# Kernel tuning notes

Measured on AMD Instinct MI355X. Metric: run time of the kernel, lower is better.

The kernel has to match this reference:

```python
import jax, jax.numpy as jnp
import numpy as np

UNITS = 64

def _tri_indices(u):
    # pairs (a,b) with b>=a in row-major order == tf.boolean_mask(product_mask1)
    pairs = [(a, b) for a in range(u) for b in range(a, u)]
    ia = np.array([p[0] for p in pairs], np.int32)
    ib = np.array([p[1] for p in pairs], np.int32)
    # triples: for product1 index p=(a,b), keep c>=b (derived from mask2 loops)
    ip, ic = [], []
    for p, (a, b) in enumerate(pairs):
        for c in range(b, u):
            ip.append(p)
            ic.append(c)
    return ia, ib, np.array(ip, np.int32), np.array(ic, np.int32)

def setup_inputs() -> dict:
    key = jax.random.key(0)
    k0, k1, k2, k3, k4 = jax.random.split(key, 5)
    B, D, u = 4096, 66, UNITS
    nprod1 = u * (u + 1) // 2            # 2080
    nprod2 = u * (u + 1) * (u + 2) // 6  # 45760
    inputs = jax.random.normal(k0, (B, D), jnp.float32)
    fw1 = jax.random.uniform(k1, (u,), jnp.float32, 0.0, 2.0 * np.pi * 40.0)
    fw2 = jax.random.normal(k2, (u,), jnp.float32) * 0.05
    fb1 = jax.random.normal(k3, (u,), jnp.float32) * 0.05
    wo = jax.random.normal(k4, (u + nprod1 + nprod2, u), jnp.float32) * 0.05
    return {"inputs": inputs, "fw1": fw1, "fw2": fw2, "fb1": fb1, "wo": wo}

def reference(inputs, fw1, fw2, fb1, wo):
    u = fw1.shape[0]
    ia, ib, ip, ic = _tri_indices(u)
    # Fourier features: cos(x * w1 + b1) * w2,  [B, u]
    f = jnp.cos(inputs[:, :u] * fw1 + fb1) * fw2
    # quadratic upper-triangular products, [B, nprod1] (gather instead of dense outer+mask)
    p1 = f[:, ia] * f[:, ib]
    # cubic products c>=b>=a, [B, nprod2]
    p2 = p1[:, ip] * f[:, ic]
    comb = jnp.concatenate([f, p1, p2], axis=1)  # [B, u+nprod1+nprod2]
    pad = jnp.zeros((inputs.shape[0], inputs.shape[1] - u), inputs.dtype)
    return jnp.concatenate([comb @ wo, pad], axis=1) + inputs
```

## Files before the change

kernel.cpp:

```cpp
#include <hip/hip_runtime.h>
#include <hip/hip_bf16.h>

#define NB      4096
#define ND      66
#define NSTEPP  1792
#define KS      64
#define CH      28
#define MB      32
#define FS      72

#define SBLK    NSTEPP
#define FBLK    (NB*FS/256)
#define PBLK    32

typedef __attribute__((ext_vector_type(8))) _Float16 f16x8;
typedef __attribute__((ext_vector_type(4))) _Float16 f16x4;
typedef __attribute__((ext_vector_type(4))) float    f32x4;

__device__ __attribute__((aligned(16))) _Float16 g_f[NB * FS];
__device__ __attribute__((aligned(16))) _Float16 g_woTi[(size_t)(NSTEPP + 1) * 2048];
__device__ __attribute__((aligned(16))) _Float16 g_part[(size_t)KS * MB * 8192];

__constant__ int c_bb[8] = {0, 48, 204, 532, 1096, 1960, 3188, 4844};

__device__ inline unsigned octet_desc(int o) {
    int t = 0;
#pragma unroll
    for (int i = 1; i < 8; ++i) t += (o >= c_bb[i]);
    int li = o - c_bb[t];
    int P = 8 * t + 8, T = P * (P + 1) / 2;
    int s0, s1;
    if (li == 0)       { s0 = 64; s1 = 64; }
    else if (li <= P)  { s0 = li - 1; s1 = 64; }
    else if (li <= P + T) {
        int r = li - P - 1, a = 0;
        while (r >= P - a) { r -= P - a; ++a; }
        s0 = a; s1 = a + r;
    } else             { s0 = 65; s1 = 65; }
    return (unsigned)s0 | ((unsigned)s1 << 8) | ((unsigned)(8 * t) << 16);
}

__global__ void k_prep(const float* __restrict__ inp, const float* __restrict__ fw1,
                       const float* __restrict__ fw2, const float* __restrict__ fb1,
                       const float* __restrict__ wo, float* __restrict__ out) {
    const int bid = blockIdx.x, tid = threadIdx.x;
    if (bid < SBLK) {
        __shared__ unsigned sd[4];
        if (tid < 4) sd[tid] = octet_desc(bid * 4 + tid);
        __syncthreads();
        const int q = tid >> 6, gg = (tid >> 4) & 3, rl = tid & 15;
        const unsigned d = sd[gg];
        const int s0 = d & 255, s1 = (d >> 8) & 255, cb = d >> 16;
        const int n = q * 16 + rl;
        f16x8 v;
        if (s0 == 64) {
#pragma unroll
            for (int j = 0; j < 8; ++j) v[j] = (_Float16)wo[(cb + j) * 64 + n];
        } else if (s0 < 64 && s1 == 64) {
            int base = 64 + s0 * (129 - s0) / 2 + (cb - s0);
#pragma unroll
            for (int j = 0; j < 8; ++j)
                v[j] = (cb + j >= s0) ? (_Float16)wo[(base + j) * 64 + n] : (_Float16)0.f;
        } else if (s0 < 64) {
            int a = s0, b = s1;
            int TP = 45760 - (64 - a) * (65 - a) * (66 - a) / 6;
            int RB = b * (129 - b) / 2 - a * (129 - a) / 2;
            int base = 2144 + TP + RB + (cb - b);
#pragma unroll
            for (int j = 0; j < 8; ++j)
                v[j] = (cb + j >= b) ? (_Float16)wo[(base + j) * 64 + n] : (_Float16)0.f;
        } else {
#pragma unroll
            for (int j = 0; j < 8; ++j) v[j] = (_Float16)0.f;
        }
        *(f16x8*)(g_woTi + (size_t)bid * 2048 + tid * 8) = v;
    } else if (bid < SBLK + FBLK) {
        int i = (bid - SBLK) * 256 + tid;
        int r = i / FS, c = i - r * FS;
        float v;
        if (c < 64)       v = cosf(inp[r * ND + c] * fw1[c] + fb1[c]) * fw2[c];
        else if (c == 64) v = 1.0f;
        else              v = 0.0f;
        g_f[i] = (_Float16)v;
    } else {
        int i = (bid - SBLK - FBLK) * 256 + tid;
        int r = i >> 1, c = 64 + (i & 1);
        out[r * ND + c] = inp[r * ND + c];
    }
}

__global__ __launch_bounds__(128, 4) void k_gemm() {
    __shared__ __attribute__((aligned(16))) _Float16 fl[128 * FS];
    __shared__ __attribute__((aligned(16))) unsigned ldescT[4 * 32];
    const int mb = blockIdx.x, ks = blockIdx.y, tid = threadIdx.x;
    const int s0c = ks * CH;

    {
        const uint4* src = (const uint4*)(g_f + (size_t)mb * 128 * FS);
        uint4* dst = (uint4*)fl;
        for (int e = tid; e < 128 * FS * 2 / 16; e += 128) dst[e] = src[e];
        {
            int gg = tid >> 5, s = tid & 31;
            ldescT[tid] = (s < CH) ? octet_desc((s0c + s) * 4 + gg) : (65u | (65u << 8));
        }
    }
    __syncthreads();

    const int wave = tid >> 6, lane = tid & 63, rl = lane & 15, g = lane >> 4;
    const _Float16* fr0 = fl + (wave * 64 +  0 + rl) * FS;
    const _Float16* fr1 = fl + (wave * 64 + 16 + rl) * FS;
    const _Float16* fr2 = fl + (wave * 64 + 32 + rl) * FS;
    const _Float16* fr3 = fl + (wave * 64 + 48 + rl) * FS;

    f32x4 acc[4][4];
#pragma unroll
    for (int a = 0; a < 4; ++a)
#pragma unroll
        for (int q = 0; q < 4; ++q) acc[a][q] = f32x4{0.f, 0.f, 0.f, 0.f};

    f16x8 c0{}, c1{}, c2{}, c3{};
    _Float16 fa0 = 0, fa1 = 0, fa2 = 0, fa3 = 0;
    int cbPrev = -1, siPrev = -1;

    const _Float16* bptr = g_woTi + (size_t)s0c * 2048 + lane * 8;
    f16x8 B0 = *(const f16x8*)(bptr +    0);
    f16x8 B1 = *(const f16x8*)(bptr +  512);
    f16x8 B2 = *(const f16x8*)(bptr + 1024);
    f16x8 B3 = *(const f16x8*)(bptr + 1536);
    bptr += 2048;

#define STEP(dv)                                                               \
    {                                                                          \
        const int si0 = (dv) & 255, si1 = ((dv) >> 8) & 255;                   \
        const int cb = __builtin_amdgcn_readfirstlane((dv) >> 16);             \
        if (__any(si0 != siPrev)) {                                            \
            siPrev = si0;                                                      \
            fa0 = fr0[si0]; fa1 = fr1[si0]; fa2 = fr2[si0]; fa3 = fr3[si0];    \
        }                                                                      \
        if (cb != cbPrev) {                                                    \
            cbPrev = cb;                                                       \
            c0 = *(const f16x8*)(fr0 + cb); c1 = *(const f16x8*)(fr1 + cb);    \
            c2 = *(const f16x8*)(fr2 + cb); c3 = *(const f16x8*)(fr3 + cb);    \
        }                                                                      \
        f16x8 nB0 = *(const f16x8*)(bptr +    0);                              \
        f16x8 nB1 = *(const f16x8*)(bptr +  512);                              \
        f16x8 nB2 = *(const f16x8*)(bptr + 1024);                              \
        f16x8 nB3 = *(const f16x8*)(bptr + 1536);                              \
        bptr += 2048;                                                          \
        const _Float16 p0 = fa0 * fr0[si1], p1 = fa1 * fr1[si1];               \
        const _Float16 p2 = fa2 * fr2[si1], p3 = fa3 * fr3[si1];               \
        const f16x8 a0 = c0 * p0, a1 = c1 * p1, a2 = c2 * p2, a3 = c3 * p3;    \
        acc[0][0] = __builtin_amdgcn_mfma_f32_16x16x32_f16(a0, B0, acc[0][0], 0, 0, 0); \
        acc[0][1] = __builtin_amdgcn_mfma_f32_16x16x32_f16(a0, B1, acc[0][1], 0, 0, 0); \
        acc[0][2] = __builtin_amdgcn_mfma_f32_16x16x32_f16(a0, B2, acc[0][2], 0, 0, 0); \
        acc[0][3] = __builtin_amdgcn_mfma_f32_16x16x32_f16(a0, B3, acc[0][3], 0, 0, 0); \
        acc[1][0] = __builtin_amdgcn_mfma_f32_16x16x32_f16(a1, B0, acc[1][0], 0, 0, 0); \
        acc[1][1] = __builtin_amdgcn_mfma_f32_16x16x32_f16(a1, B1, acc[1][1], 0, 0, 0); \
        acc[1][2] = __builtin_amdgcn_mfma_f32_16x16x32_f16(a1, B2, acc[1][2], 0, 0, 0); \
        acc[1][3] = __builtin_amdgcn_mfma_f32_16x16x32_f16(a1, B3, acc[1][3], 0, 0, 0); \
        acc[2][0] = __builtin_amdgcn_mfma_f32_16x16x32_f16(a2, B0, acc[2][0], 0, 0, 0); \
        acc[2][1] = __builtin_amdgcn_mfma_f32_16x16x32_f16(a2, B1, acc[2][1], 0, 0, 0); \
        acc[2][2] = __builtin_amdgcn_mfma_f32_16x16x32_f16(a2, B2, acc[2][2], 0, 0, 0); \
        acc[2][3] = __builtin_amdgcn_mfma_f32_16x16x32_f16(a2, B3, acc[2][3], 0, 0, 0); \
        acc[3][0] = __builtin_amdgcn_mfma_f32_16x16x32_f16(a3, B0, acc[3][0], 0, 0, 0); \
        acc[3][1] = __builtin_amdgcn_mfma_f32_16x16x32_f16(a3, B1, acc[3][1], 0, 0, 0); \
        acc[3][2] = __builtin_amdgcn_mfma_f32_16x16x32_f16(a3, B2, acc[3][2], 0, 0, 0); \
        acc[3][3] = __builtin_amdgcn_mfma_f32_16x16x32_f16(a3, B3, acc[3][3], 0, 0, 0); \
        B0 = nB0; B1 = nB1; B2 = nB2; B3 = nB3;                                \
    }

    const unsigned* dT = ldescT + g * 32;
#pragma unroll 1
    for (int s2 = 0; s2 < CH; s2 += 2) {
        uint2 dd = *(const uint2*)(dT + s2);
        STEP(dd.x);
        STEP(dd.y);
    }
#undef STEP

    _Float16* pp = g_part + ((size_t)ks * MB + mb) * 8192 + wave * 4096;
#pragma unroll
    for (int a = 0; a < 4; ++a)
#pragma unroll
        for (int q = 0; q < 4; ++q) {
            f16x4 v;
            v[0] = (_Float16)acc[a][q][0]; v[1] = (_Float16)acc[a][q][1];
            v[2] = (_Float16)acc[a][q][2]; v[3] = (_Float16)acc[a][q][3];
            *(f16x4*)(pp + (a * 4 + q) * 256 + lane * 4) = v;
        }
}

__global__ void k_reduce(const float* __restrict__ inp, float* __restrict__ out) {
    int t = blockIdx.x * 256 + threadIdx.x;
    int c = t & 63, rg = t >> 6;
    int mb = rg >> 5, wave = (rg >> 4) & 1, a = (rg >> 2) & 3, g = rg & 3;
    int q = c >> 4, rl = c & 15, lane = g * 16 + rl;
    int rbase = mb * 128 + wave * 64 + a * 16 + g * 4;
    float acc[4];
#pragma unroll
    for (int i2 = 0; i2 < 4; ++i2) acc[i2] = inp[(rbase + i2) * ND + c];
    const _Float16* pp = g_part + (size_t)mb * 8192 + wave * 4096
                       + (a * 4 + q) * 256 + lane * 4;
#pragma unroll
    for (int ks = 0; ks < KS; ++ks) {
        const f16x4 p = *(const f16x4*)(pp + (size_t)ks * MB * 8192);
#pragma unroll
        for (int i2 = 0; i2 < 4; ++i2) acc[i2] += (float)p[i2];
    }
#pragma unroll
    for (int i2 = 0; i2 < 4; ++i2) out[(rbase + i2) * ND + c] = acc[i2];
}

extern "C" void kernel_launch(void* const* d_in, const int* in_sizes, int n_in,
                              void* d_out, int out_size, void* d_ws, size_t ws_size,
                              hipStream_t stream) {
    const float* inp = (const float*)d_in[0];
    const float* fw1 = (const float*)d_in[1];
    const float* fw2 = (const float*)d_in[2];
    const float* fb1 = (const float*)d_in[3];
    const float* wo  = (const float*)d_in[4];
    float* out = (float*)d_out;

    k_prep<<<SBLK + FBLK + PBLK, 256, 0, stream>>>(inp, fw1, fw2, fb1, wo, out);
    k_gemm<<<dim3(MB, KS), 128, 0, stream>>>();
    k_reduce<<<256, 256, 0, stream>>>(inp, out);
}
```

Baseline: 49.15 us.

## Halve K-split count and coalesce weight repack through shared-memory transpose

The GEMM K-split count drops from 64 to 32, with each block handling twice as many steps. This halves the fp16 partial-sum buffer written and later reduced, at the cost of fewer blocks in flight. The weight repack in the prep kernel now reads each row of wo as two contiguous float4 loads per thread instead of strided scalar loads. It then transposes the data in shared memory before one coalesced 16-byte store. The per-step descriptor table and the padded weight buffer are enlarged to match the longer chunk.

New measurement: 49.23 us. About the same (+0.2%).

```diff
diff --git a/kernel.cpp b/kernel.cpp
--- a/kernel.cpp
+++ b/kernel.cpp
@@ -4,8 +4,8 @@
 #define NB      4096
 #define ND      66
 #define NSTEPP  1792
-#define KS      64
-#define CH      28
+#define KS      32
+#define CH      56
 #define MB      32
 #define FS      72
 
@@ -18,7 +18,7 @@
 typedef __attribute__((ext_vector_type(4))) float    f32x4;
 
 __device__ __attribute__((aligned(16))) _Float16 g_f[NB * FS];
-__device__ __attribute__((aligned(16))) _Float16 g_woTi[(size_t)(NSTEPP + 1) * 2048];
+__device__ __attribute__((aligned(16))) _Float16 g_woTi[(size_t)(NSTEPP + 8) * 2048];
 __device__ __attribute__((aligned(16))) _Float16 g_part[(size_t)KS * MB * 8192];
 
 __constant__ int c_bb[8] = {0, 48, 204, 532, 1096, 1960, 3188, 4844};
@@ -45,35 +45,49 @@
                        const float* __restrict__ wo, float* __restrict__ out) {
     const int bid = blockIdx.x, tid = threadIdx.x;
     if (bid < SBLK) {
-        __shared__ unsigned sd[4];
-        if (tid < 4) sd[tid] = octet_desc(bid * 4 + tid);
+        __shared__ int sbrow[4], sminj[4];
+        __shared__ __attribute__((aligned(16))) _Float16 sw[2048];
+        if (tid < 4) {
+            unsigned d = octet_desc(bid * 4 + tid);
+            int s0 = d & 255, s1 = (d >> 8) & 255, cb = d >> 16;
+            int brow, minj = 0;
+            if (s0 == 64) {
+                brow = cb;
+            } else if (s0 < 64 && s1 == 64) {
+                brow = 64 + s0 * (129 - s0) / 2 + (cb - s0);
+                minj = (s0 > cb) ? s0 - cb : 0;
+            } else if (s0 < 64) {
+                int a = s0, b = s1;
+                int TP = 45760 - (64 - a) * (65 - a) * (66 - a) / 6;
+                int RB = b * (129 - b) / 2 - a * (129 - a) / 2;
+                brow = 2144 + TP + RB + (cb - b);
+                minj = (b > cb) ? b - cb : 0;
+            } else brow = -1;
+            sbrow[tid] = brow; sminj[tid] = minj;
+        }
         __syncthreads();
-        const int q = tid >> 6, gg = (tid >> 4) & 3, rl = tid & 15;
-        const unsigned d = sd[gg];
-        const int s0 = d & 255, s1 = (d >> 8) & 255, cb = d >> 16;
-        const int n = q * 16 + rl;
-        f16x8 v;
-        if (s0 == 64) {
-#pragma unroll
-            for (int j = 0; j < 8; ++j) v[j] = (_Float16)wo[(cb + j) * 64 + n];
-        } else if (s0 < 64 && s1 == 64) {
-            int base = 64 + s0 * (129 - s0) / 2 + (cb - s0);
-#pragma unroll
-            for (int j = 0; j < 8; ++j)
-                v[j] = (cb + j >= s0) ? (_Float16)wo[(base + j) * 64 + n] : (_Float16)0.f;
-        } else if (s0 < 64) {
-            int a = s0, b = s1;
-            int TP = 45760 - (64 - a) * (65 - a) * (66 - a) / 6;
-            int RB = b * (129 - b) / 2 - a * (129 - a) / 2;
-            int base = 2144 + TP + RB + (cb - b);
-#pragma unroll
-            for (int j = 0; j < 8; ++j)
-                v[j] = (cb + j >= b) ? (_Float16)wo[(base + j) * 64 + n] : (_Float16)0.f;
+        const int o = tid >> 6, l = tid & 63;
+        const int j = l >> 3, n0 = 8 * (l & 7);
+        const int brow = sbrow[o], minj = sminj[o];
+        f16x8 hv;
+        if (brow >= 0 && j >= minj) {
+            const float4 w0 = *(const float4*)(wo + (size_t)(brow + j) * 64 + n0);
+            const float4 w1 = *(const float4*)(wo + (size_t)(brow + j) * 64 + n0 + 4);
+            hv[0] = (_Float16)w0.x; hv[1] = (_Float16)w0.y;
+            hv[2] = (_Float16)w0.z; hv[3] = (_Float16)w0.w;
+            hv[4] = (_Float16)w1.x; hv[5] = (_Float16)w1.y;
+            hv[6] = (_Float16)w1.z; hv[7] = (_Float16)w1.w;
         } else {
 #pragma unroll
-            for (int j = 0; j < 8; ++j) v[j] = (_Float16)0.f;
-        }
-        *(f16x8*)(g_woTi + (size_t)bid * 2048 + tid * 8) = v;
+            for (int k = 0; k < 8; ++k) hv[k] = (_Float16)0.f;
+        }
+#pragma unroll
+        for (int k = 0; k < 8; ++k) {
+            int n = n0 + k;
+            sw[(n >> 4) * 512 + o * 128 + (n & 15) * 8 + j] = hv[k];
+        }
+        __syncthreads();
+        *(f16x8*)(g_woTi + (size_t)bid * 2048 + tid * 8) = *(const f16x8*)(sw + tid * 8);
     } else if (bid < SBLK + FBLK) {
         int i = (bid - SBLK) * 256 + tid;
         int r = i / FS, c = i - r * FS;
@@ -91,7 +105,7 @@
 
 __global__ __launch_bounds__(128, 4) void k_gemm() {
     __shared__ __attribute__((aligned(16))) _Float16 fl[128 * FS];
-    __shared__ __attribute__((aligned(16))) unsigned ldescT[4 * 32];
+    __shared__ __attribute__((aligned(16))) unsigned ldescT[4 * 64];
     const int mb = blockIdx.x, ks = blockIdx.y, tid = threadIdx.x;
     const int s0c = ks * CH;
 
@@ -99,9 +113,9 @@
         const uint4* src = (const uint4*)(g_f + (size_t)mb * 128 * FS);
         uint4* dst = (uint4*)fl;
         for (int e = tid; e < 128 * FS * 2 / 16; e += 128) dst[e] = src[e];
-        {
-            int gg = tid >> 5, s = tid & 31;
-            ldescT[tid] = (s < CH) ? octet_desc((s0c + s) * 4 + gg) : (65u | (65u << 8));
+        for (int e = tid; e < 4 * 64; e += 128) {
+            int gg = e >> 6, s = e & 63;
+            ldescT[e] = (s < CH) ? octet_desc((s0c + s) * 4 + gg) : (65u | (65u << 8));
         }
     }
     __syncthreads();
@@ -169,7 +183,7 @@
         B0 = nB0; B1 = nB1; B2 = nB2; B3 = nB3;                                \
     }
 
-    const unsigned* dT = ldescT + g * 32;
+    const unsigned* dT = ldescT + g * 64;
 #pragma unroll 1
     for (int s2 = 0; s2 < CH; s2 += 2) {
         uint2 dd = *(const uint2*)(dT + s2);
```
